# Performance work log

Hardware: AMD Instinct MI355X
Metric: run time of the kernel (lower is better)

## Reference

```python
import jax, jax.numpy as jnp
import numpy as np
import math

D_MODEL = 1024
NUM_HEADS = 16
HEAD_DIM = D_MODEL // NUM_HEADS
EPS = 1e-6
ROPE_BASE = 10000.0


def _rope_cos_sin(seq_len, dim, dtype):
    inv_freq = 1.0 / (ROPE_BASE ** (jnp.arange(0, dim, 2, dtype=jnp.float32) / dim))
    t = jnp.arange(seq_len, dtype=jnp.float32)
    freqs = jnp.outer(t, inv_freq)                 # [s, dim/2]
    emb = jnp.concatenate([freqs, freqs], axis=-1)  # [s, dim]
    return jnp.cos(emb).astype(dtype), jnp.sin(emb).astype(dtype)


def _rotate_half(x):
    x1, x2 = jnp.split(x, 2, axis=-1)
    return jnp.concatenate([-x2, x1], axis=-1)


def setup_inputs() -> dict:
    key = jax.random.key(0)
    k1, k2, k3 = jax.random.split(key, 3)
    b, s = 2, 2048
    x = jax.random.normal(k1, (b, s, D_MODEL), dtype=jnp.float32)
    norm_w = jnp.ones((D_MODEL,), dtype=jnp.float32)
    qkv_w = jax.random.normal(k2, (3 * D_MODEL, D_MODEL), dtype=jnp.float32) * (1.0 / math.sqrt(D_MODEL))
    qkv_b = jnp.zeros((3 * D_MODEL,), dtype=jnp.float32)
    proj_w = jax.random.normal(k3, (D_MODEL, D_MODEL), dtype=jnp.float32) * (1.0 / math.sqrt(D_MODEL))
    proj_b = jnp.zeros((D_MODEL,), dtype=jnp.float32)
    return {"x": x, "norm_w": norm_w, "qkv_w": qkv_w, "qkv_b": qkv_b,
            "proj_w": proj_w, "proj_b": proj_b}


def reference(x, norm_w, qkv_w, qkv_b, proj_w, proj_b):
    b, s, d = x.shape
    # RMSNorm (pre-LN)
    xn = x * jax.lax.rsqrt(jnp.mean(x * x, axis=-1, keepdims=True) + EPS) * norm_w
    # Fused QKV
    qkv = jnp.einsum('bsd,ed->bse', xn, qkv_w) + qkv_b
    q, k, v = jnp.split(qkv, 3, axis=-1)
    # [b, h, s, hd]
    def shape(t):
        return t.reshape(b, s, NUM_HEADS, HEAD_DIM).transpose(0, 2, 1, 3)
    q, k, v = shape(q), shape(k), shape(v)
    # RoPE on head_dim
    cos, sin = _rope_cos_sin(s, HEAD_DIM, x.dtype)  # [s, hd]
    q = q * cos + _rotate_half(q) * sin
    k = k * cos + _rotate_half(k) * sin
    # Naive causal attention
    scale = 1.0 / math.sqrt(HEAD_DIM)
    scores = jnp.einsum('bhqd,bhkd->bhqk', q, k) * scale
    causal = jnp.tril(jnp.ones((s, s), dtype=bool))
    scores = jnp.where(causal, scores, -jnp.inf)
    attn = jax.nn.softmax(scores, axis=-1)
    y = jnp.einsum('bhqk,bhkd->bhqd', attn, v)
    y = y.transpose(0, 2, 1, 3).reshape(b, s, d)
    return jnp.einsum('bsd,ed->bse', y, proj_w) + proj_b
```

## Files before the change

### kernel.cpp

```cpp
#include <hip/hip_runtime.h>
#include <cstdint>
#include <cstddef>

#define NB 2
#define NS 2048
#define ND 1024
#define NH 16
#define HD 64
#define ROWS 4096
#define E3 3072

using bf16 = __bf16;
typedef __attribute__((ext_vector_type(4))) __bf16 bf16x4;
typedef __attribute__((ext_vector_type(8))) __bf16 bf16x8;
typedef __attribute__((ext_vector_type(4))) float f32x4;

__device__ __forceinline__ f32x4 mfma16(bf16x8 a, bf16x8 b, f32x4 c) {
    return __builtin_amdgcn_mfma_f32_16x16x32_bf16(a, b, c, 0, 0, 0);
}

__device__ __forceinline__ void gll16(const bf16* src, bf16* lds) {
    __builtin_amdgcn_global_load_lds(
        (const __attribute__((address_space(1))) void*)src,
        (__attribute__((address_space(3))) void*)lds, 16, 0, 0);
}

__global__ __launch_bounds__(256) void cast_f32_bf16(const float* __restrict__ in,
                                                     bf16* __restrict__ out, int n) {
    int i = (blockIdx.x * 256 + threadIdx.x) * 4;
    if (i + 3 < n) {
        float4 v = *(const float4*)(in + i);
        bf16x4 o;
        o[0] = (bf16)v.x; o[1] = (bf16)v.y; o[2] = (bf16)v.z; o[3] = (bf16)v.w;
        *(bf16x4*)(out + i) = o;
    }
}

__global__ __launch_bounds__(256) void rmsnorm_cast(const float* __restrict__ x,
                                                    const float* __restrict__ w,
                                                    bf16* __restrict__ xn) {
    int row = blockIdx.x;
    int tid = threadIdx.x;
    const float* xr = x + (size_t)row * ND;
    float4 v = ((const float4*)xr)[tid];
    float ss = v.x*v.x + v.y*v.y + v.z*v.z + v.w*v.w;
    #pragma unroll
    for (int m = 32; m >= 1; m >>= 1) ss += __shfl_xor(ss, m);
    __shared__ float wsum[4];
    if ((tid & 63) == 0) wsum[tid >> 6] = ss;
    __syncthreads();
    float total = wsum[0] + wsum[1] + wsum[2] + wsum[3];
    float scale = rsqrtf(total * (1.0f / ND) + 1e-6f);
    float4 wv = ((const float4*)w)[tid];
    bf16x4 o;
    o[0] = (bf16)(v.x * scale * wv.x);
    o[1] = (bf16)(v.y * scale * wv.y);
    o[2] = (bf16)(v.z * scale * wv.z);
    o[3] = (bf16)(v.w * scale * wv.w);
    ((bf16x4*)(xn + (size_t)row * ND))[tid] = o;
}

__global__ __launch_bounds__(256) void gemm_qkv_rope(const bf16* __restrict__ A,
                                                     const bf16* __restrict__ Bm,
                                                     const float* __restrict__ bias,
                                                     bf16* __restrict__ Qb,
                                                     bf16* __restrict__ Kb,
                                                     bf16* __restrict__ Vraw) {
    const int K = ND;
    __shared__ bf16 Asm[128 * 32];
    __shared__ bf16 Bsm[128 * 32];
    const int tid = threadIdx.x;
    const int wave = tid >> 6, lane = tid & 63;
    const int quad = lane >> 4, l15 = lane & 15;
    const int row0 = blockIdx.x * 128, col0 = blockIdx.y * 128;
    const int wr = (wave >> 1) * 64, wc = (wave & 1) * 64;
    const int srow = lane >> 2;
    const int scol = (lane & 3) * 8;

    f32x4 acc[4][4] = {};

    for (int k0 = 0; k0 < K; k0 += 32) {
        #pragma unroll
        for (int i = 0; i < 2; ++i) {
            int r = wave * 32 + i * 16;
            gll16(A + (size_t)(row0 + r + srow) * K + k0 + scol, Asm + r * 32);
            gll16(Bm + (size_t)(col0 + r + srow) * K + k0 + scol, Bsm + r * 32);
        }
        __syncthreads();
        bf16x8 af[4], bff[4];
        #pragma unroll
        for (int t = 0; t < 4; ++t) {
            af[t]  = *(const bf16x8*)(Asm + (wr + t * 16 + l15) * 32 + quad * 8);
            bff[t] = *(const bf16x8*)(Bsm + (wc + t * 16 + l15) * 32 + quad * 8);
        }
        #pragma unroll
        for (int mt = 0; mt < 4; ++mt)
            #pragma unroll
            for (int nt = 0; nt < 4; ++nt)
                acc[mt][nt] = mfma16(af[mt], bff[nt], acc[mt][nt]);
        __syncthreads();
    }

    float bb[4];
    #pragma unroll
    for (int nt = 0; nt < 4; ++nt) bb[nt] = bias[col0 + wc + nt * 16 + l15];

    const int region = col0 >> 10;
    if (region == 2) {
        int cv = col0 - 2048 + wc;
        #pragma unroll
        for (int mt = 0; mt < 4; ++mt)
            #pragma unroll
            for (int r = 0; r < 4; ++r) {
                int row = row0 + wr + mt * 16 + quad * 4 + r;
                #pragma unroll
                for (int nt = 0; nt < 4; ++nt)
                    Vraw[(size_t)row * ND + cv + nt * 16 + l15] = (bf16)(acc[mt][nt][r] + bb[nt]);
            }
    } else {
        const float scale = (region == 0) ? 0.125f : 1.0f;
        bf16* Ob = (region == 0) ? Qb : Kb;
        const int h = ((col0 + wc) & 1023) >> 6;
        float freq0 = powf(10000.0f, -(float)l15 * (1.0f / 32.0f));
        float freq1 = powf(10000.0f, -(float)(16 + l15) * (1.0f / 32.0f));
        #pragma unroll
        for (int mt = 0; mt < 4; ++mt) {
            #pragma unroll
            for (int r = 0; r < 4; ++r) {
                int row = row0 + wr + mt * 16 + quad * 4 + r;
                int s = row & (NS - 1);
                int b = row >> 11;
                float sn0, c0, sn1, c1;
                sincosf((float)s * freq0, &sn0, &c0);
                sincosf((float)s * freq1, &sn1, &c1);
                size_t obase = ((size_t)(b * NH + h) * NS + s) * 64;
                #pragma unroll
                for (int nt = 0; nt < 4; ++nt) {
                    float v  = acc[mt][nt][r] + bb[nt];
                    float vp = acc[mt][nt ^ 2][r] + bb[nt ^ 2];
                    float cc = (nt & 1) ? c1 : c0;
                    float ss = (nt & 1) ? sn1 : sn0;
                    float res = (nt < 2) ? (v * cc - vp * ss) : (v * cc + vp * ss);
                    Ob[obase + nt * 16 + l15] = (bf16)(res * scale);
                }
            }
        }
    }
}

__global__ __launch_bounds__(256) void gemm_bt_f32(const bf16* __restrict__ A,
                                                   const bf16* __restrict__ Bm,
                                                   const float* __restrict__ bias,
                                                   float* __restrict__ C,
                                                   int M, int N, int K) {
    __shared__ bf16 Asm[128 * 32];
    __shared__ bf16 Bsm[128 * 32];
    const int tid = threadIdx.x;
    const int wave = tid >> 6, lane = tid & 63;
    const int quad = lane >> 4, l15 = lane & 15;
    const int row0 = blockIdx.x * 128, col0 = blockIdx.y * 128;
    const int wr = (wave >> 1) * 64, wc = (wave & 1) * 64;
    const int srow = lane >> 2;
    const int scol = (lane & 3) * 8;

    f32x4 acc[4][4] = {};

    for (int k0 = 0; k0 < K; k0 += 32) {
        #pragma unroll
        for (int i = 0; i < 2; ++i) {
            int r = wave * 32 + i * 16;
            gll16(A + (size_t)(row0 + r + srow) * K + k0 + scol, Asm + r * 32);
            gll16(Bm + (size_t)(col0 + r + srow) * K + k0 + scol, Bsm + r * 32);
        }
        __syncthreads();
        bf16x8 af[4], bff[4];
        #pragma unroll
        for (int t = 0; t < 4; ++t) {
            af[t]  = *(const bf16x8*)(Asm + (wr + t * 16 + l15) * 32 + quad * 8);
            bff[t] = *(const bf16x8*)(Bsm + (wc + t * 16 + l15) * 32 + quad * 8);
        }
        #pragma unroll
        for (int mt = 0; mt < 4; ++mt)
            #pragma unroll
            for (int nt = 0; nt < 4; ++nt)
                acc[mt][nt] = mfma16(af[mt], bff[nt], acc[mt][nt]);
        __syncthreads();
    }

    #pragma unroll
    for (int nt = 0; nt < 4; ++nt) {
        int col = col0 + wc + nt * 16 + l15;
        float bv = bias[col];
        #pragma unroll
        for (int mt = 0; mt < 4; ++mt) {
            int row = row0 + wr + mt * 16 + quad * 4;
            #pragma unroll
            for (int r = 0; r < 4; ++r)
                C[(size_t)(row + r) * N + col] = acc[mt][nt][r] + bv;
        }
    }
}

__global__ __launch_bounds__(256) void transpose_v(const bf16* __restrict__ Vraw,
                                                   bf16* __restrict__ Vt) {
    __shared__ bf16 t[64][65];
    int bid = blockIdx.x;
    int st = bid & 31;
    int bh = bid >> 5;
    int h = bh & 15, b = bh >> 4;
    int s0 = st * 64;
    int d = threadIdx.x & 63, i0 = threadIdx.x >> 6;
    for (int i = i0; i < 64; i += 4)
        t[i][d] = Vraw[(size_t)(b * NS + s0 + i) * ND + h * 64 + d];
    __syncthreads();
    int j = threadIdx.x & 63, d0 = threadIdx.x >> 6;
    int jp = (j & 32) | ((j & 12) << 1) | ((j & 16) >> 2) | (j & 3);
    for (int dd = d0; dd < 64; dd += 4)
        Vt[((size_t)bh * 64 + dd) * NS + s0 + jp] = t[j][dd];
}

__global__ __launch_bounds__(256) void attn(const bf16* __restrict__ Q,
                                            const bf16* __restrict__ K,
                                            const bf16* __restrict__ Vt,
                                            bf16* __restrict__ Y) {
    __shared__ bf16 Ksm[4096];
    __shared__ bf16 Vsm[4096];
    int bid = blockIdx.x;
    int g = bid >> 5;
    int bh = bid & 31;
    int qt = (g < 8) ? (15 - g) : (g - 8);
    int tid = threadIdx.x;
    int wave = tid >> 6, lane = tid & 63;
    int quad = lane >> 4, l15 = lane & 15;
    int q0 = qt * 128 + wave * 32;
    const bf16* Qh = Q + (size_t)bh * NS * 64;
    const bf16* Kh = K + (size_t)bh * NS * 64;
    const bf16* Vh = Vt + (size_t)bh * 64 * NS;
    const float NEG_INF = -__builtin_inff();

    const int srow = tid >> 3;
    const int sx   = (tid & 7) ^ (srow & 7);
    const bf16* sK = Kh + (size_t)srow * 64 + sx * 8;
    const bf16* sV = Vh + (size_t)srow * NS + sx * 8;
    bf16* dK = Ksm + wave * 512;
    bf16* dV = Vsm + wave * 512;

    const int x7 = l15 & 7;
    const bf16* pk0 = Ksm + l15 * 64 + ((quad) ^ x7) * 8;
    const bf16* pk1 = Ksm + l15 * 64 + ((4 + quad) ^ x7) * 8;
    const bf16* pv0 = Vsm + l15 * 64 + ((quad) ^ x7) * 8;
    const bf16* pv1 = Vsm + l15 * 64 + ((4 + quad) ^ x7) * 8;

    bf16x8 bq[2][2];
    #pragma unroll
    for (int t = 0; t < 2; ++t)
        #pragma unroll
        for (int hh = 0; hh < 2; ++hh)
            bq[t][hh] = *(const bf16x8*)(Qh + (size_t)(q0 + t * 16 + l15) * 64 + hh * 32 + quad * 8);

    f32x4 o[2][4] = {};
    float lsum[2] = {0.f, 0.f};

    const int ncb = 2 * (qt + 1);
    for (int c = 0; c < ncb; ++c) {
        const int kb = c * 64;
        const bf16* kSrc = sK + (size_t)kb * 64;
        const bf16* vSrc = sV + kb;
        gll16(kSrc, dK);
        gll16(kSrc + 32 * 64, dK + 2048);
        gll16(vSrc, dV);
        gll16(vSrc + (size_t)32 * NS, dV + 2048);
        __syncthreads();

        #pragma unroll
        for (int ksub = 0; ksub < 2; ++ksub) {
            const int kbs = kb + ksub * 32;
            if (kbs <= q0) {
                const int kh0 = ksub * 2;
                bf16x8 ak00 = *(const bf16x8*)(pk0 + kh0 * 1024);
                bf16x8 ak01 = *(const bf16x8*)(pk1 + kh0 * 1024);
                bf16x8 ak10 = *(const bf16x8*)(pk0 + (kh0 + 1) * 1024);
                bf16x8 ak11 = *(const bf16x8*)(pk1 + (kh0 + 1) * 1024);
                const bf16* pv = ksub ? pv1 : pv0;
                bf16x8 vf0 = *(const bf16x8*)(pv);
                bf16x8 vf1 = *(const bf16x8*)(pv + 1024);
                bf16x8 vf2 = *(const bf16x8*)(pv + 2048);
                bf16x8 vf3 = *(const bf16x8*)(pv + 3072);
                const bool masked = (kbs == q0);
                #pragma unroll
                for (int t = 0; t < 2; ++t) {
                    f32x4 sh0 = {}, sh1 = {};
                    sh0 = mfma16(ak00, bq[t][0], sh0);
                    sh0 = mfma16(ak01, bq[t][1], sh0);
                    sh1 = mfma16(ak10, bq[t][0], sh1);
                    sh1 = mfma16(ak11, bq[t][1], sh1);
                    if (masked) {
                        int qy = q0 + t * 16 + l15;
                        #pragma unroll
                        for (int r = 0; r < 4; ++r) {
                            if (kbs + quad * 4 + r > qy)      sh0[r] = NEG_INF;
                            if (kbs + 16 + quad * 4 + r > qy) sh1[r] = NEG_INF;
                        }
                    }
                    bf16x8 pa;
                    float ls = 0.f;
                    #pragma unroll
                    for (int j = 0; j < 4; ++j) {
                        float p0 = __expf(sh0[j]);
                        float p1 = __expf(sh1[j]);
                        ls += p0 + p1;
                        pa[j] = (bf16)p0;
                        pa[4 + j] = (bf16)p1;
                    }
                    lsum[t] += ls;
                    o[t][0] = mfma16(pa, vf0, o[t][0]);
                    o[t][1] = mfma16(pa, vf1, o[t][1]);
                    o[t][2] = mfma16(pa, vf2, o[t][2]);
                    o[t][3] = mfma16(pa, vf3, o[t][3]);
                }
            }
        }
        __syncthreads();
    }

    int b = bh >> 4, h = bh & 15;
    #pragma unroll
    for (int t = 0; t < 2; ++t) {
        float red = lsum[t];
        red += __shfl_xor(red, 16);
        red += __shfl_xor(red, 32);
        #pragma unroll
        for (int r = 0; r < 4; ++r) {
            float il = 1.0f / __shfl(red, quad * 4 + r);
            size_t row = (size_t)(b * NS + q0 + t * 16 + quad * 4 + r);
            #pragma unroll
            for (int nt = 0; nt < 4; ++nt)
                Y[row * ND + h * 64 + nt * 16 + l15] = (bf16)(o[t][nt][r] * il);
        }
    }
}

extern "C" void kernel_launch(void* const* d_in, const int* in_sizes, int n_in,
                              void* d_out, int out_size, void* d_ws, size_t ws_size,
                              hipStream_t stream) {
    const float* x      = (const float*)d_in[0];
    const float* norm_w = (const float*)d_in[1];
    const float* qkv_w  = (const float*)d_in[2];
    const float* qkv_b  = (const float*)d_in[3];
    const float* proj_w = (const float*)d_in[4];
    const float* proj_b = (const float*)d_in[5];
    float* out = (float*)d_out;

    char* ws = (char*)d_ws;
    size_t off = 0;
    bf16* xn   = (bf16*)(ws + off); off += (size_t)ROWS * ND * 2;
    bf16* wq   = (bf16*)(ws + off); off += (size_t)E3 * ND * 2;
    bf16* wp   = (bf16*)(ws + off); off += (size_t)ND * ND * 2;
    bf16* Qb   = (bf16*)(ws + off); off += (size_t)NB * NH * NS * HD * 2;
    bf16* Kb   = (bf16*)(ws + off); off += (size_t)NB * NH * NS * HD * 2;
    bf16* Vraw = (bf16*)(ws + off); off += (size_t)ROWS * ND * 2;
    bf16* Vt   = (bf16*)(ws + off); off += (size_t)NB * NH * HD * NS * 2;
    bf16* Y    = (bf16*)(ws + off); off += (size_t)ROWS * ND * 2;

    cast_f32_bf16<<<3072, 256, 0, stream>>>(qkv_w, wq, E3 * ND);
    cast_f32_bf16<<<1024, 256, 0, stream>>>(proj_w, wp, ND * ND);
    rmsnorm_cast<<<ROWS, 256, 0, stream>>>(x, norm_w, xn);
    gemm_qkv_rope<<<dim3(ROWS / 128, E3 / 128), 256, 0, stream>>>(xn, wq, qkv_b, Qb, Kb, Vraw);
    transpose_v<<<NB * NH * (NS / 64), 256, 0, stream>>>(Vraw, Vt);
    attn<<<NB * NH * (NS / 128), 256, 0, stream>>>(Qb, Kb, Vt, Y);
    gemm_bt_f32<<<dim3(ROWS / 128, ND / 128), 256, 0, stream>>>(Y, wp, proj_b, out, ROWS, ND, ND);
}
```

Measured before the change: 201.5 us.

## Precompute RoPE sin/cos table and halve attention query tile per block

Adds a small kernel that precomputes the RoPE cos/sin values per position into a float4 table, so the QKV GEMM epilogue loads them instead of calling powf and sincosf per row. The attention kernel is reworked so each block covers 64 queries (16 per wave) instead of 128, doubling the grid. This is meant to improve occupancy and load balance on the causal triangle. The cost is more K/V tile reloads per query and less reuse of each loaded K/V fragment across query sub-tiles.

```diff
diff --git a/kernel.cpp b/kernel.cpp
--- a/kernel.cpp
+++ b/kernel.cpp
@@ -23,6 +23,17 @@
     __builtin_amdgcn_global_load_lds(
         (const __attribute__((address_space(1))) void*)src,
         (__attribute__((address_space(3))) void*)lds, 16, 0, 0);
+}
+
+__global__ __launch_bounds__(256) void rope_table(float4* __restrict__ tab) {
+    int idx = blockIdx.x * 256 + threadIdx.x;
+    int s = idx >> 4, j = idx & 15;
+    float f0 = powf(10000.0f, -(float)j * (1.0f / 32.0f));
+    float f1 = powf(10000.0f, -(float)(j + 16) * (1.0f / 32.0f));
+    float sn0, c0, sn1, c1;
+    sincosf((float)s * f0, &sn0, &c0);
+    sincosf((float)s * f1, &sn1, &c1);
+    tab[idx] = make_float4(c0, sn0, c1, sn1);
 }
 
 __global__ __launch_bounds__(256) void cast_f32_bf16(const float* __restrict__ in,
@@ -63,6 +74,7 @@
 __global__ __launch_bounds__(256) void gemm_qkv_rope(const bf16* __restrict__ A,
                                                      const bf16* __restrict__ Bm,
                                                      const float* __restrict__ bias,
+                                                     const float4* __restrict__ tab,
                                                      bf16* __restrict__ Qb,
                                                      bf16* __restrict__ Kb,
                                                      bf16* __restrict__ Vraw) {
@@ -121,8 +133,6 @@
         const float scale = (region == 0) ? 0.125f : 1.0f;
         bf16* Ob = (region == 0) ? Qb : Kb;
         const int h = ((col0 + wc) & 1023) >> 6;
-        float freq0 = powf(10000.0f, -(float)l15 * (1.0f / 32.0f));
-        float freq1 = powf(10000.0f, -(float)(16 + l15) * (1.0f / 32.0f));
         #pragma unroll
         for (int mt = 0; mt < 4; ++mt) {
             #pragma unroll
@@ -130,16 +140,14 @@
                 int row = row0 + wr + mt * 16 + quad * 4 + r;
                 int s = row & (NS - 1);
                 int b = row >> 11;
-                float sn0, c0, sn1, c1;
-                sincosf((float)s * freq0, &sn0, &c0);
-                sincosf((float)s * freq1, &sn1, &c1);
+                float4 cs = tab[s * 16 + l15];
                 size_t obase = ((size_t)(b * NH + h) * NS + s) * 64;
                 #pragma unroll
                 for (int nt = 0; nt < 4; ++nt) {
                     float v  = acc[mt][nt][r] + bb[nt];
                     float vp = acc[mt][nt ^ 2][r] + bb[nt ^ 2];
-                    float cc = (nt & 1) ? c1 : c0;
-                    float ss = (nt & 1) ? sn1 : sn0;
+                    float cc = (nt & 1) ? cs.z : cs.x;
+                    float ss = (nt & 1) ? cs.w : cs.y;
                     float res = (nt < 2) ? (v * cc - vp * ss) : (v * cc + vp * ss);
                     Ob[obase + nt * 16 + l15] = (bf16)(res * scale);
                 }
@@ -228,11 +236,11 @@
     int bid = blockIdx.x;
     int g = bid >> 5;
     int bh = bid & 31;
-    int qt = (g < 8) ? (15 - g) : (g - 8);
+    int qt = (g < 16) ? (31 - g) : (g - 16);
     int tid = threadIdx.x;
     int wave = tid >> 6, lane = tid & 63;
     int quad = lane >> 4, l15 = lane & 15;
-    int q0 = qt * 128 + wave * 32;
+    int q0 = qt * 64 + wave * 16;
     const bf16* Qh = Q + (size_t)bh * NS * 64;
     const bf16* Kh = K + (size_t)bh * NS * 64;
     const bf16* Vh = Vt + (size_t)bh * 64 * NS;
@@ -251,17 +259,13 @@
     const bf16* pv0 = Vsm + l15 * 64 + ((quad) ^ x7) * 8;
     const bf16* pv1 = Vsm + l15 * 64 + ((4 + quad) ^ x7) * 8;
 
-    bf16x8 bq[2][2];
-    #pragma unroll
-    for (int t = 0; t < 2; ++t)
-        #pragma unroll
-        for (int hh = 0; hh < 2; ++hh)
-            bq[t][hh] = *(const bf16x8*)(Qh + (size_t)(q0 + t * 16 + l15) * 64 + hh * 32 + quad * 8);
-
-    f32x4 o[2][4] = {};
-    float lsum[2] = {0.f, 0.f};
-
-    const int ncb = 2 * (qt + 1);
+    bf16x8 bq0 = *(const bf16x8*)(Qh + (size_t)(q0 + l15) * 64 + quad * 8);
+    bf16x8 bq1 = *(const bf16x8*)(Qh + (size_t)(q0 + l15) * 64 + 32 + quad * 8);
+
+    f32x4 o0 = {}, o1 = {}, o2 = {}, o3 = {};
+    float lsum = 0.f;
+
+    const int ncb = qt + 1;
     for (int c = 0; c < ncb; ++c) {
         const int kb = c * 64;
         const bf16* kSrc = sK + (size_t)kb * 64;
@@ -275,7 +279,7 @@
         #pragma unroll
         for (int ksub = 0; ksub < 2; ++ksub) {
             const int kbs = kb + ksub * 32;
-            if (kbs <= q0) {
+            if (kbs < q0 + 16) {
                 const int kh0 = ksub * 2;
                 bf16x8 ak00 = *(const bf16x8*)(pk0 + kh0 * 1024);
                 bf16x8 ak01 = *(const bf16x8*)(pk1 + kh0 * 1024);
@@ -286,57 +290,52 @@
                 bf16x8 vf1 = *(const bf16x8*)(pv + 1024);
                 bf16x8 vf2 = *(const bf16x8*)(pv + 2048);
                 bf16x8 vf3 = *(const bf16x8*)(pv + 3072);
-                const bool masked = (kbs == q0);
+
+                f32x4 sh0 = {}, sh1 = {};
+                sh0 = mfma16(ak00, bq0, sh0);
+                sh0 = mfma16(ak01, bq1, sh0);
+                sh1 = mfma16(ak10, bq0, sh1);
+                sh1 = mfma16(ak11, bq1, sh1);
+                if (kbs + 32 > q0) {
+                    int qy = q0 + l15;
+                    #pragma unroll
+                    for (int r = 0; r < 4; ++r) {
+                        if (kbs + quad * 4 + r > qy)      sh0[r] = NEG_INF;
+                        if (kbs + 16 + quad * 4 + r > qy) sh1[r] = NEG_INF;
+                    }
+                }
+                bf16x8 pa;
+                float ls = 0.f;
                 #pragma unroll
-                for (int t = 0; t < 2; ++t) {
-                    f32x4 sh0 = {}, sh1 = {};
-                    sh0 = mfma16(ak00, bq[t][0], sh0);
-                    sh0 = mfma16(ak01, bq[t][1], sh0);
-                    sh1 = mfma16(ak10, bq[t][0], sh1);
-                    sh1 = mfma16(ak11, bq[t][1], sh1);
-                    if (masked) {
-                        int qy = q0 + t * 16 + l15;
-                        #pragma unroll
-                        for (int r = 0; r < 4; ++r) {
-                            if (kbs + quad * 4 + r > qy)      sh0[r] = NEG_INF;
-                            if (kbs + 16 + quad * 4 + r > qy) sh1[r] = NEG_INF;
-                        }
-                    }
-                    bf16x8 pa;
-                    float ls = 0.f;
-                    #pragma unroll
-                    for (int j = 0; j < 4; ++j) {
-                        float p0 = __expf(sh0[j]);
-                        float p1 = __expf(sh1[j]);
-                        ls += p0 + p1;
-                        pa[j] = (bf16)p0;
-                        pa[4 + j] = (bf16)p1;
-                    }
-                    lsum[t] += ls;
-                    o[t][0] = mfma16(pa, vf0, o[t][0]);
-                    o[t][1] = mfma16(pa, vf1, o[t][1]);
-                    o[t][2] = mfma16(pa, vf2, o[t][2]);
-                    o[t][3] = mfma16(pa, vf3, o[t][3]);
+                for (int j = 0; j < 4; ++j) {
+                    float p0 = __expf(sh0[j]);
+                    float p1 = __expf(sh1[j]);
+                    ls += p0 + p1;
+                    pa[j] = (bf16)p0;
+                    pa[4 + j] = (bf16)p1;
                 }
+                lsum += ls;
+                o0 = mfma16(pa, vf0, o0);
+                o1 = mfma16(pa, vf1, o1);
+                o2 = mfma16(pa, vf2, o2);
+                o3 = mfma16(pa, vf3, o3);
             }
         }
         __syncthreads();
     }
 
     int b = bh >> 4, h = bh & 15;
+    float red = lsum;
+    red += __shfl_xor(red, 16);
+    red += __shfl_xor(red, 32);
+    f32x4 ov[4] = {o0, o1, o2, o3};
     #pragma unroll
-    for (int t = 0; t < 2; ++t) {
-        float red = lsum[t];
-        red += __shfl_xor(red, 16);
-        red += __shfl_xor(red, 32);
-        #pragma unroll
-        for (int r = 0; r < 4; ++r) {
-            float il = 1.0f / __shfl(red, quad * 4 + r);
-            size_t row = (size_t)(b * NS + q0 + t * 16 + quad * 4 + r);
-            #pragma unroll
-            for (int nt = 0; nt < 4; ++nt)
-                Y[row * ND + h * 64 + nt * 16 + l15] = (bf16)(o[t][nt][r] * il);
-        }
+    for (int r = 0; r < 4; ++r) {
+        float il = 1.0f / __shfl(red, quad * 4 + r);
+        size_t row = (size_t)(b * NS + q0 + quad * 4 + r);
+        #pragma unroll
+        for (int nt = 0; nt < 4; ++nt)
+            Y[row * ND + h * 64 + nt * 16 + l15] = (bf16)(ov[nt][r] * il);
     }
 }
 
@@ -353,20 +352,22 @@
 
     char* ws = (char*)d_ws;
     size_t off = 0;
-    bf16* xn   = (bf16*)(ws + off); off += (size_t)ROWS * ND * 2;
-    bf16* wq   = (bf16*)(ws + off); off += (size_t)E3 * ND * 2;
-    bf16* wp   = (bf16*)(ws + off); off += (size_t)ND * ND * 2;
-    bf16* Qb   = (bf16*)(ws + off); off += (size_t)NB * NH * NS * HD * 2;
-    bf16* Kb   = (bf16*)(ws + off); off += (size_t)NB * NH * NS * HD * 2;
-    bf16* Vraw = (bf16*)(ws + off); off += (size_t)ROWS * ND * 2;
-    bf16* Vt   = (bf16*)(ws + off); off += (size_t)NB * NH * HD * NS * 2;
-    bf16* Y    = (bf16*)(ws + off); off += (size_t)ROWS * ND * 2;
-
+    bf16* xn    = (bf16*)(ws + off); off += (size_t)ROWS * ND * 2;
+    bf16* wq    = (bf16*)(ws + off); off += (size_t)E3 * ND * 2;
+    bf16* wp    = (bf16*)(ws + off); off += (size_t)ND * ND * 2;
+    bf16* Qb    = (bf16*)(ws + off); off += (size_t)NB * NH * NS * HD * 2;
+    bf16* Kb    = (bf16*)(ws + off); off += (size_t)NB * NH * NS * HD * 2;
+    bf16* Vraw  = (bf16*)(ws + off); off += (size_t)ROWS * ND * 2;
+    bf16* Vt    = (bf16*)(ws + off); off += (size_t)NB * NH * HD * NS * 2;
+    bf16* Y     = (bf16*)(ws + off); off += (size_t)ROWS * ND * 2;
+    float4* tab = (float4*)(ws + off); off += (size_t)NS * 16 * sizeof(float4);
+
+    rope_table<<<NS * 16 / 256, 256, 0, stream>>>(tab);
     cast_f32_bf16<<<3072, 256, 0, stream>>>(qkv_w, wq, E3 * ND);
     cast_f32_bf16<<<1024, 256, 0, stream>>>(proj_w, wp, ND * ND);
     rmsnorm_cast<<<ROWS, 256, 0, stream>>>(x, norm_w, xn);
-    gemm_qkv_rope<<<dim3(ROWS / 128, E3 / 128), 256, 0, stream>>>(xn, wq, qkv_b, Qb, Kb, Vraw);
+    gemm_qkv_rope<<<dim3(ROWS / 128, E3 / 128), 256, 0, stream>>>(xn, wq, qkv_b, tab, Qb, Kb, Vraw);
     transpose_v<<<NB * NH * (NS / 64), 256, 0, stream>>>(Vraw, Vt);
-    attn<<<NB * NH * (NS / 128), 256, 0, stream>>>(Qb, Kb, Vt, Y);
+    attn<<<NB * NH * (NS / 64), 256, 0, stream>>>(Qb, Kb, Vt, Y);
     gemm_bt_f32<<<dim3(ROWS / 128, ND / 128), 256, 0, stream>>>(Y, wp, proj_b, out, ROWS, ND, ND);
 }
```

Result: no change. 201.9 us (+0.2%).
